# Performance work log

Hardware: AMD Instinct MI355X
Metric: run time of the kernel (lower is better)

Reference implementation:

```python
import jax, jax.numpy as jnp
import numpy as np

REC_W, COMMIT_W, SMOOTH_W = 1.0, 1.0, 0.1
CHUNK_SIZE = 10
W_DEC = 5
EPS = 1e-12


def conv1d(x, w, b):
    # x: (B, Cin, T), w: (Cout, Cin, K) -> 'same' padding, stride 1
    p = (w.shape[-1] - 1) // 2
    y = jax.lax.conv_general_dilated(x, w, (1,), [(p, p)],
                                     dimension_numbers=("NCH", "OIH", "NCH"))
    return y + b[None, :, None]


def adaptive_avg_pool1d(x, out_size):
    # PyTorch adaptive_avg_pool1d: bin i averages input[start:end],
    # start = floor(i*In/Out), end = ceil((i+1)*In/Out). Via cumsum.
    In = x.shape[-1]
    i = jnp.arange(out_size)
    start = (i * In) // out_size
    end = -((-(i + 1) * In) // out_size)
    cs = jnp.concatenate([jnp.zeros_like(x[..., :1]), jnp.cumsum(x, -1)], -1)
    return (cs[..., end] - cs[..., start]) / (end - start).astype(x.dtype)


def interp_linear(x, out_size):
    # F.interpolate(mode='linear', align_corners=False)
    In = x.shape[-1]
    scale = In / out_size
    src = jnp.maximum((jnp.arange(out_size) + 0.5) * scale - 0.5, 0.0)
    i0 = jnp.floor(src).astype(jnp.int32)
    i1 = jnp.minimum(i0 + 1, In - 1)
    frac = (src - i0).astype(x.dtype)
    return x[..., i0] * (1 - frac) + x[..., i1] * frac


def rotate_to(src, tgt):
    # rotation trick (vector-quantize-pytorch): Householder-style rotation of src onto tgt direction
    sg = jax.lax.stop_gradient
    ns = jnp.linalg.norm(src, axis=-1, keepdims=True)
    nt = jnp.linalg.norm(tgt, axis=-1, keepdims=True)
    u = src / (ns + EPS)
    q = tgt / (nt + EPS)
    w = sg((u + q) / (jnp.linalg.norm(u + q, axis=-1, keepdims=True) + EPS))
    e = src
    rotated = (e
               - 2 * jnp.sum(e * w, -1, keepdims=True) * w
               + 2 * jnp.sum(e * sg(u), -1, keepdims=True) * q)
    return rotated * sg(nt / (ns + EPS))


def residual_vq(x, codebooks):
    # x: (B, T, D); codebooks: (Q, K, D)
    sg = jax.lax.stop_gradient
    residual = x
    quantized_out = jnp.zeros_like(x)
    codes, losses = [], []
    for qi in range(codebooks.shape[0]):
        cb = codebooks[qi]                                # (K, D)
        d = (jnp.sum(residual * residual, -1, keepdims=True)
             - 2.0 * jnp.einsum("btd,kd->btk", residual, cb)
             + jnp.sum(cb * cb, -1)[None, None, :])       # (B, T, K)
        idx = jnp.argmin(d, axis=-1)                      # (B, T)
        quant = cb[idx]                                   # (B, T, D)
        losses.append(jnp.mean((sg(quant) - residual) ** 2))  # commitment loss
        quant_r = rotate_to(residual, quant)
        quantized_out = quantized_out + quant_r
        residual = residual - sg(quant_r)
        codes.append(idx)
    return quantized_out, jnp.stack(codes, -1), jnp.stack(losses)


def setup_inputs() -> dict:
    key = jax.random.key(0)
    ks = jax.random.split(key, 16)
    B, T = 16, 8000
    input_dim, hidden, latent, K, Q = 2, 512, 128, 1024, 4
    s = 0.02
    return {
        "traj_xy": jax.random.normal(ks[0], (B, input_dim, T), jnp.float32),
        "masks": jnp.ones((B, T), jnp.bool_),
        "enc1_w": s * jax.random.normal(ks[1], (hidden, input_dim * CHUNK_SIZE, 3), jnp.float32),
        "enc1_b": jnp.zeros((hidden,), jnp.float32),
        "enc2a_w": s * jax.random.normal(ks[2], (hidden, hidden, 5), jnp.float32),
        "enc2a_b": jnp.zeros((hidden,), jnp.float32),
        "enc2b_w": s * jax.random.normal(ks[3], (latent, hidden, 7), jnp.float32),
        "enc2b_b": jnp.zeros((latent,), jnp.float32),
        "dec1_w": s * jax.random.normal(ks[4], (hidden, latent + Q, 5), jnp.float32),
        "dec1_b": jnp.zeros((hidden,), jnp.float32),
        "dec2_w": s * jax.random.normal(ks[5], (latent, hidden, 3), jnp.float32),
        "dec2_b": jnp.zeros((latent,), jnp.float32),
        "codebooks": jax.random.normal(ks[6], (Q, K, latent), jnp.float32),
    }


def _forward(traj_xy, enc1_w, enc1_b, enc2a_w, enc2a_b, enc2b_w, enc2b_b,
             dec1_w, dec1_b, dec2_w, dec2_b, codebooks):
    B, D, T = traj_xy.shape
    Tn = T // CHUNK_SIZE
    # (B, D, T) -> (B, D*chunk, T/chunk)
    x = traj_xy.reshape(B, D, Tn, CHUNK_SIZE).transpose(0, 2, 1, 3).reshape(B, Tn, D * CHUNK_SIZE)
    x = x.transpose(0, 2, 1)
    z = jax.nn.relu(conv1d(x, enc1_w, enc1_b))
    z = adaptive_avg_pool1d(z, T // 2)
    z = interp_linear(z, T)
    z = jax.nn.relu(conv1d(z, enc2a_w, enc2a_b))
    z = conv1d(z, enc2b_w, enc2b_b)           # (B, latent, T)
    z_e = z.transpose(0, 2, 1)                # (B, T, latent)

    quantized, codes, vq_losses = residual_vq(z_e, codebooks)
    vq_loss = jnp.mean(vq_losses)

    codes_z = codes.transpose(0, 2, 1).astype(z.dtype)   # (B, Q, T)
    quant = quantized.transpose(0, 2, 1)                 # (B, latent, T)

    # chunked decoder loop, vectorized: starts t = 0, W, ..., T-2W
    Wd = W_DEC
    count = (T - 2 * Wd) // Wd + 1                       # = T/W - 1
    span = count * Wd                                    # = T - W
    Lq, Qn = quant.shape[1], codes_z.shape[1]
    past = quant[:, :, :span].reshape(B, Lq, count, Wd)
    cq = codes_z[:, :, :span].reshape(B, Qn, count, Wd)
    dec_in = jnp.concatenate([past, cq], axis=1)         # (B, Lq+Q, count, W)
    dec_in = dec_in.transpose(0, 2, 1, 3).reshape(B * count, Lq + Qn, Wd)
    h = jax.nn.relu(conv1d(dec_in, dec1_w, dec1_b))
    dec_out = conv1d(h, dec2_w, dec2_b)                  # (B*count, latent, W)
    true_chunk = quant[:, :, Wd:Wd + span].reshape(B, Lq, count, Wd)
    true_chunk = true_chunk.transpose(0, 2, 1, 3).reshape(B * count, Lq, Wd)
    recon_loss = jnp.mean((dec_out - true_chunk) ** 2)   # mean of equal-size per-chunk MSEs

    c0 = codes[:, :, 0]
    smooth_loss = jnp.mean((c0[:, 1:] != c0[:, :-1]).astype(z.dtype))

    loss = recon_loss * REC_W + vq_loss * COMMIT_W + smooth_loss * SMOOTH_W
    return codes, loss, recon_loss, vq_loss, smooth_loss


def reference(traj_xy, masks, enc1_w, enc1_b, enc2a_w, enc2a_b, enc2b_w, enc2b_b,
              dec1_w, dec1_b, dec2_w, dec2_b, codebooks):
    return _forward(traj_xy, enc1_w, enc1_b, enc2a_w, enc2a_b, enc2b_w, enc2b_b,
                    dec1_w, dec1_b, dec2_w, dec2_b, codebooks)
```

## Files before the change

kernel.cpp:

```cpp
#include <hip/hip_runtime.h>
#include <cstdint>
#include <cstddef>

#define B_     16
#define T_     8000
#define TN_    800
#define HID_   512
#define L_     128
#define KCB_   1024
#define Q_     4
#define COUNT_ 1599
#define NC_    (B_*COUNT_)
#define NTOK_  (B_*T_)
#define EPSF   1e-12

#define KP1_   672
#define NN1_   2560
#define KP2_   2560
#define NN2_   640

#define ZROWS_ 8072
#define ZROWU_ 1024
#define Z2ROWS_ 8072ull
#define Z2ROWU_ 1024ull
// ... 327 lines not shown
        #pragma unroll
        for (int j = 0; j < 4; ++j) acc[i][j] = (f32x4){0.f,0.f,0.f,0.f};

    for (int ci0 = 0; ci0 < 512; ci0 += 32){
        __syncthreads();
        for (int idx = tid; idx < 1056; idx += 256){
            int row = idx >> 3, rem = idx & 7, pl = rem >> 2, qo = rem & 3;
            *(uint4*)&SH[pl*4224 + row*32 + qo*8] =
                *(const uint4*)&Zb[(size_t)(t0 + row)*ZROWU_ + (size_t)pl*512 + ci0 + qo*8];
        }
        for (int u = 0; u < 5; ++u){
            if (u) __syncthreads();
            #pragma unroll
            for (int p = 0; p < 4; ++p){
                int idx = p*256 + tid;
                int n = idx >> 3, rem = idx & 7, pl = rem >> 2, qo = rem & 3;
                *(uint4*)&SH[8448 + pl*4096 + n*32 + qo*8] =
                    *(const uint4*)&Wp[((size_t)(co0+n)*2 + pl)*2560 + u*512 + ci0 + qo*8];
            }
            __syncthreads();
            s16x8 w[2][4], z[2][4];
            #pragma unroll
            for (int pl = 0; pl < 2; ++pl)
                #pragma unroll
                for (int mi = 0; mi < 4; ++mi)
                    w[pl][mi] = *(const s16x8*)&SH[8448 + pl*4096 + (wr*64 + mi*16 + lr)*32 + lg*8];
            #pragma unroll
            for (int pl = 0; pl < 2; ++pl)
                #pragma unroll
                for (int ni = 0; ni < 4; ++ni)
                    z[pl][ni] = *(const s16x8*)&SH[pl*4224 + (wc*64 + ni*16 + lr + u)*32 + lg*8];
            #pragma unroll
            for (int mi = 0; mi < 4; ++mi)
                #pragma unroll
                for (int ni = 0; ni < 4; ++ni){
                    f32x4 c = acc[mi][ni];
                    c = MFMA16(w[0][mi], z[0][ni], c);
                    c = MFMA16(w[0][mi], z[1][ni], c);
                    c = MFMA16(w[1][mi], z[0][ni], c);
                    acc[mi][ni] = c;
                }
        }
    }
    unsigned short* Zo = z2t + (size_t)lb*(Z2ROWS_*Z2ROWU_);
    #pragma unroll
    for (int pl = 0; pl < 2; ++pl){
        __syncthreads();
        #pragma unroll
        for (int mi = 0; mi < 4; ++mi){
            int cb = wr*64 + mi*16 + lg*4;
            #pragma unroll
            for (int ni = 0; ni < 4; ++ni){
                int tl = wc*64 + ni*16 + lr;
                #pragma unroll
                for (int r = 0; r < 4; ++r){
                    float v = fmaxf(acc[mi][ni][r] + bias[co0 + cb + r], 0.f);
                    unsigned short h, l; bsplit(v, h, l);
                    SH[tl*136 + cb + r] = pl ? l : h;
                }
            }
        }
        __syncthreads();
        int tl = tid >> 1, half = tid & 1;
        if (t0 + tl < T_){
            uint4* dst = (uint4*)&Zo[((size_t)(t0 + tl + 3))*Z2ROWU_ + (size_t)pl*512 + co0 + half*64];
            const uint4* src = (const uint4*)&SH[tl*136 + half*64];
            #pragma unroll
            for (int e = 0; e < 8; ++e) dst[e] = src[e];
        }
    }
}

__global__ __launch_bounds__(256) void k_mconv2b(const unsigned short* __restrict__ Z2,
                                                 const unsigned short* __restrict__ Wp,
                                                 const float* __restrict__ bias,
                                                 float* __restrict__ ze){
    __shared__ unsigned short SH[12672];
    int lb = blockIdx.y;
    int t0 = blockIdx.x * 64;
    int tid = threadIdx.x;
    int lane = tid & 63, wid = tid >> 6;
    int lr = lane & 15, lg = lane >> 4;
    const unsigned short* Zb = Z2 + (size_t)lb*(Z2ROWS_*Z2ROWU_);
    f32x4 acc[2][4];
    #pragma unroll
    for (int i = 0; i < 2; ++i)
        #pragma unroll
        for (int j = 0; j < 4; ++j) acc[i][j] = (f32x4){0.f,0.f,0.f,0.f};

    for (int ci0 = 0; ci0 < 512; ci0 += 32){
        __syncthreads();
        for (int idx = tid; idx < 560; idx += 256){
            int row = idx >> 3, rem = idx & 7, pl = rem >> 2, qo = rem & 3;
            *(uint4*)&SH[pl*2240 + row*32 + qo*8] =
                *(const uint4*)&Zb[(size_t)(t0 + row)*Z2ROWU_ + (size_t)pl*512 + ci0 + qo*8];
        }
        for (int u = 0; u < 7; ++u){
            if (u) __syncthreads();
            #pragma unroll
            for (int p = 0; p < 4; ++p){
                int idx = p*256 + tid;
                int n = idx >> 3, rem = idx & 7, pl = rem >> 2, qo = rem & 3;
                *(uint4*)&SH[4480 + pl*4096 + n*32 + qo*8] =
                    *(const uint4*)&Wp[((size_t)n*2 + pl)*3584 + u*512 + ci0 + qo*8];
            }
            __syncthreads();
            s16x8 w[2][2], z[2][4];
            #pragma unroll
            for (int pl = 0; pl < 2; ++pl)
                #pragma unroll
                for (int mi = 0; mi < 2; ++mi)
                    w[pl][mi] = *(const s16x8*)&SH[4480 + pl*4096 + (wid*32 + mi*16 + lr)*32 + lg*8];
            #pragma unroll
            for (int pl = 0; pl < 2; ++pl)
                #pragma unroll
                for (int ni = 0; ni < 4; ++ni)
                    z[pl][ni] = *(const s16x8*)&SH[pl*2240 + (ni*16 + lr + u)*32 + lg*8];
            #pragma unroll
            for (int mi = 0; mi < 2; ++mi)
                #pragma unroll
                for (int ni = 0; ni < 4; ++ni){
                    f32x4 c = acc[mi][ni];
                    c = MFMA16(w[0][mi], z[0][ni], c);
                    c = MFMA16(w[0][mi], z[1][ni], c);
                    c = MFMA16(w[1][mi], z[0][ni], c);
                    acc[mi][ni] = c;
                }
        }
    }
    #pragma unroll
    for (int mi = 0; mi < 2; ++mi){
        int cb = wid*32 + mi*16 + lg*4;
        float4 bv = *(const float4*)&bias[cb];
        #pragma unroll
        for (int ni = 0; ni < 4; ++ni){
            int t = t0 + ni*16 + lr;
            float4 o;
            o.x = acc[mi][ni][0] + bv.x;
            o.y = acc[mi][ni][1] + bv.y;
            o.z = acc[mi][ni][2] + bv.z;
            o.w = acc[mi][ni][3] + bv.w;
            *(float4*)&ze[((size_t)lb*T_ + t)*L_ + cb] = o;
        }
    }
}

__global__ __launch_bounds__(256) void k_mgemm1(const unsigned short* __restrict__ Ap,
                                                const unsigned short* __restrict__ Bp,
                                                const float* __restrict__ bias,
                                                unsigned short* __restrict__ Hp){
    __shared__ unsigned short AL[2][128][40];
    __shared__ unsigned short BL[2][128][40];
    int m0 = blockIdx.x * 128, n0 = blockIdx.y * 128;
    int tid = threadIdx.x;
    int lane = tid & 63, wid = tid >> 6;
    int wr = wid >> 1, wc = wid & 1;
    int lr = lane & 15, lg = lane >> 4;
    f32x4 acc[4][4];
    #pragma unroll
    for (int i = 0; i < 4; ++i)
        #pragma unroll
        for (int j = 0; j < 4; ++j) acc[i][j] = (f32x4){0.f,0.f,0.f,0.f};

    for (int kb = 0; kb < KP1_; kb += 32){
        __syncthreads();
        #pragma unroll
        for (int p = 0; p < 4; ++p){
            int slot = p*256 + tid;
            int m = slot >> 3, pl = (slot >> 2) & 1, q = slot & 3;
            uint4 v = *(const uint4*)&Ap[((size_t)(m0+m)*2 + pl)*KP1_ + kb + q*8];
            *(uint4*)&AL[pl][m][q*8] = v;
        }
        #pragma unroll
        for (int p = 0; p < 4; ++p){
            int slot = p*256 + tid;
            int n = slot >> 3, pl = (slot >> 2) & 1, q = slot & 3;
            uint4 v = *(const uint4*)&Bp[((size_t)(n0+n)*2 + pl)*KP1_ + kb + q*8];
            *(uint4*)&BL[pl][n][q*8] = v;
        }
        __syncthreads();
        s16x8 a[2][4], b[2][4];
        #pragma unroll
        for (int pl = 0; pl < 2; ++pl)
            #pragma unroll
            for (int mi = 0; mi < 4; ++mi)
                a[pl][mi] = *(const s16x8*)&AL[pl][wr*64 + mi*16 + lr][lg*8];
        #pragma unroll
        for (int pl = 0; pl < 2; ++pl)
            #pragma unroll
            for (int ni = 0; ni < 4; ++ni)
                b[pl][ni] = *(const s16x8*)&BL[pl][wc*64 + ni*16 + lr][lg*8];
        #pragma unroll
        for (int mi = 0; mi < 4; ++mi)
            #pragma unroll
            for (int ni = 0; ni < 4; ++ni){
                f32x4 c = acc[mi][ni];
                c = MFMA16(a[0][mi], b[0][ni], c);
                c = MFMA16(a[0][mi], b[1][ni], c);
                c = MFMA16(a[1][mi], b[0][ni], c);
                acc[mi][ni] = c;
            }
    }
    #pragma unroll
    for (int mi = 0; mi < 4; ++mi){
        int mbase = m0 + wr*64 + mi*16 + lg*4;
        #pragma unroll
        for (int ni = 0; ni < 4; ++ni){
            int n = n0 + wc*64 + ni*16 + lr;
            float bv = bias[n/5];
            #pragma unroll
            for (int r = 0; r < 4; ++r){
                float v = fmaxf(acc[mi][ni][r] + bv, 0.f);
                unsigned short h, l; bsplit(v, h, l);
                size_t m = (size_t)(mbase + r);
                Hp[(m*2 + 0)*NN1_ + n] = h;
                Hp[(m*2 + 1)*NN1_ + n] = l;
            }
        }
    }
}

__global__ __launch_bounds__(256) void k_mgemm2rec(const unsigned short* __restrict__ Ap,
                                                   const unsigned short* __restrict__ Bp,
                                                   const float* __restrict__ bias,
                                                   const float* __restrict__ zeq, float* __restrict__ scal,
                                                   int M, int m0g){
    __shared__ unsigned short AL[2][128][40];
    __shared__ unsigned short BL[2][128][40];
    int m0 = blockIdx.x * 128, n0 = blockIdx.y * 128;
    int tid = threadIdx.x;
    int lane = tid & 63, wid = tid >> 6;
    int wr = wid >> 1, wc = wid & 1;
    int lr = lane & 15, lg = lane >> 4;
    f32x4 acc[4][4];
    #pragma unroll
    for (int i = 0; i < 4; ++i)
        #pragma unroll
        for (int j = 0; j < 4; ++j) acc[i][j] = (f32x4){0.f,0.f,0.f,0.f};

    for (int kb = 0; kb < KP2_; kb += 32){
        __syncthreads();
        #pragma unroll
        for (int p = 0; p < 4; ++p){
            int slot = p*256 + tid;
            int m = slot >> 3, pl = (slot >> 2) & 1, q = slot & 3;
            uint4 v = *(const uint4*)&Ap[((size_t)(m0+m)*2 + pl)*KP2_ + kb + q*8];
            *(uint4*)&AL[pl][m][q*8] = v;
        }
        #pragma unroll
        for (int p = 0; p < 4; ++p){
            int slot = p*256 + tid;
            int n = slot >> 3, pl = (slot >> 2) & 1, q = slot & 3;
            uint4 v = *(const uint4*)&Bp[((size_t)(n0+n)*2 + pl)*KP2_ + kb + q*8];
            *(uint4*)&BL[pl][n][q*8] = v;
        }
        __syncthreads();
        s16x8 a[2][4], b[2][4];
        #pragma unroll
        for (int pl = 0; pl < 2; ++pl)
            #pragma unroll
            for (int mi = 0; mi < 4; ++mi)
                a[pl][mi] = *(const s16x8*)&AL[pl][wr*64 + mi*16 + lr][lg*8];
        #pragma unroll
        for (int pl = 0; pl < 2; ++pl)
            #pragma unroll
            for (int ni = 0; ni < 4; ++ni)
                b[pl][ni] = *(const s16x8*)&BL[pl][wc*64 + ni*16 + lr][lg*8];
        #pragma unroll
        for (int mi = 0; mi < 4; ++mi)
            #pragma unroll
            for (int ni = 0; ni < 4; ++ni){
                f32x4 c = acc[mi][ni];
                c = MFMA16(a[0][mi], b[0][ni], c);
                c = MFMA16(a[0][mi], b[1][ni], c);
                c = MFMA16(a[1][mi], b[0][ni], c);
                acc[mi][ni] = c;
            }
    }
    float lsum = 0.f;
    #pragma unroll
    for (int mi = 0; mi < 4; ++mi){
        #pragma unroll
        for (int r = 0; r < 4; ++r){
            int ml = wr*64 + mi*16 + lg*4 + r;
            int mlg = m0 + ml;
            if (mlg >= M) continue;
            int gm = m0g + mlg;
            int b = gm / COUNT_, c = gm % COUNT_;
            const float* tgtB = zeq + ((size_t)b*T_ + (size_t)(c+1)*5) * L_;
            #pragma unroll
            for (int ni = 0; ni < 4; ++ni){
                int n = n0 + wc*64 + ni*16 + lr;
                int co = n / 5, t = n % 5;
                float v = acc[mi][ni][r] + bias[co];
                float d = v - tgtB[(size_t)t*L_ + co];
                lsum += d*d;
            }
        }
    }
    lsum = wred(lsum);
    if (lane == 0) atomicAdd(&scal[1024 + ((blockIdx.x*5 + blockIdx.y) & 255)], lsum);
}

#define RF(j) rf[tok*132 + sub*33 + (j)]
__global__ __launch_bounds__(256, 2) void k_vqfuse(float* __restrict__ ze,
                                                   const unsigned short* __restrict__ cbp,
                                                   const double* __restrict__ cnorm,
                                                   const float* __restrict__ cnf,
                                                   const float* __restrict__ cb,
                                                   int* __restrict__ codes,
                                                   float* __restrict__ scal){
    __shared__ unsigned short rb[2][64][136];
    __shared__ float rf[64*132];
    __shared__ float mvS[4][64][2];
    __shared__ int   miS[4][64][2];
    int tok0 = blockIdx.x * 64;
    int tid = threadIdx.x;
    int lane = tid & 63, wv = tid >> 6;
    int lr = lane & 15, lg = lane >> 4;
    int tok = tid >> 2, sub = tid & 3, dbase = sub*32;
    {
        const float* zp = &ze[((size_t)(tok0 + tok))*L_ + dbase];
        #pragma unroll
        for (int h = 0; h < 8; ++h){
            float4 v = *(const float4*)&zp[h*4];
            RF(h*4+0)=v.x; RF(h*4+1)=v.y; RF(h*4+2)=v.z; RF(h*4+3)=v.w;
        }
    }
    for (int q = 0; q < Q_; ++q){
        #pragma unroll
        for (int j = 0; j < 4; ++j){
            unsigned hp[4], lp[4];
            #pragma unroll
            for (int e = 0; e < 4; ++e){
                unsigned short h0,l0,h1,l1;
                bsplit(RF(j*8+e*2+0), h0, l0);
                bsplit(RF(j*8+e*2+1), h1, l1);
                hp[e] = (unsigned)h0 | ((unsigned)h1 << 16);
                lp[e] = (unsigned)l0 | ((unsigned)l1 << 16);
            }
            *(uint4*)&rb[0][tok][dbase + j*8] = make_uint4(hp[0],hp[1],hp[2],hp[3]);
            *(uint4*)&rb[1][tok][dbase + j*8] = make_uint4(lp[0],lp[1],lp[2],lp[3]);
        }
        __syncthreads();
        const unsigned short* cq = cbp + (size_t)q*(2*16*1024*8);
        const float* cnq = cnf + (size_t)q*KCB_;
        int code0w = wv*256;
        float m1[4], m2[4]; int i1[4], i2[4];
        #pragma unroll
        for (int t = 0; t < 4; ++t){ m1[t]=3.4e38f; m2[t]=3.4e38f; i1[t]=0x7fffffff; i2[t]=0x7fffffff; }
        for (int ch = 0; ch < 8; ++ch){
            f32x4 acc[2][4];
            #pragma unroll
            for (int i = 0; i < 2; ++i)
                #pragma unroll
                for (int j = 0; j < 4; ++j) acc[i][j] = (f32x4){0.f,0.f,0.f,0.f};
            #pragma unroll
            for (int ks = 0; ks < 4; ++ks){
                s16x8 b0[4], b1[4];
                #pragma unroll
                for (int tf = 0; tf < 4; ++tf){
                    b0[tf] = *(const s16x8*)&rb[0][tf*16 + lr][ks*32 + lg*8];
                    b1[tf] = *(const s16x8*)&rb[1][tf*16 + lr][ks*32 + lg*8];
                }
                #pragma unroll
                for (int mi = 0; mi < 2; ++mi){
                    s16x8 a0 = *(const s16x8*)&cq[((size_t)(0*16 + ks*4 + lg)*1024
                                                   + code0w + ch*32 + mi*16 + lr)*8];
                    s16x8 a1 = *(const s16x8*)&cq[((size_t)(1*16 + ks*4 + lg)*1024
                                                   + code0w + ch*32 + mi*16 + lr)*8];
                    #pragma unroll
                    for (int tf = 0; tf < 4; ++tf){
                        f32x4 c = acc[mi][tf];
                        c = MFMA16(a0, b0[tf], c);
                        c = MFMA16(a0, b1[tf], c);
                        c = MFMA16(a1, b0[tf], c);
                        acc[mi][tf] = c;
                    }
                }
            }
            #pragma unroll
            for (int mi = 0; mi < 2; ++mi){
                float4 cn4 = *(const float4*)&cnq[code0w + ch*32 + mi*16 + lg*4];
                float cnv[4] = {cn4.x, cn4.y, cn4.z, cn4.w};
                #pragma unroll
                for (int tf = 0; tf < 4; ++tf)
                    #pragma unroll
                    for (int rr = 0; rr < 4; ++rr){
                        float sc = cnv[rr] - 2.f*acc[mi][tf][rr];
                        int code = code0w + ch*32 + mi*16 + lg*4 + rr;
                        bool c1 = sc < m1[tf];
                        bool c2 = sc < m2[tf];
                        if (c1){ m2[tf]=m1[tf]; i2[tf]=i1[tf]; m1[tf]=sc; i1[tf]=code; }
                        else if (c2){ m2[tf]=sc; i2[tf]=code; }
                    }
            }
        }
        #pragma unroll
        for (int tf = 0; tf < 4; ++tf){
            float a1 = m1[tf], a2 = m2[tf]; int ai1 = i1[tf], ai2 = i2[tf];
            #pragma unroll
            for (int m = 16; m <= 32; m <<= 1){
                float o1 = __shfl_xor(a1, m), o2 = __shfl_xor(a2, m);
                int oi1 = __shfl_xor(ai1, m), oi2 = __shfl_xor(ai2, m);
                bool sw = (o1 < a1) || (o1 == a1 && oi1 < ai1);
                float w1 = sw ? o1 : a1;  int wi1 = sw ? oi1 : ai1;
                float l1 = sw ? a1 : o1;  int li1 = sw ? ai1 : oi1;
                float w2 = sw ? o2 : a2;  int wi2 = sw ? oi2 : ai2;
                bool s2 = (l1 < w2) || (l1 == w2 && li1 < wi2);
                a1 = w1; ai1 = wi1;
                a2 = s2 ? l1 : w2; ai2 = s2 ? li1 : wi2;
            }
            if (lg == 0){
                mvS[wv][tf*16 + lr][0] = a1; mvS[wv][tf*16 + lr][1] = a2;
                miS[wv][tf*16 + lr][0] = ai1; miS[wv][tf*16 + lr][1] = ai2;
            }
        }
        __syncthreads();
        float a1 = mvS[0][tok][0], a2 = mvS[0][tok][1];
        int ai1 = miS[0][tok][0], ai2 = miS[0][tok][1];
        #pragma unroll
        for (int w = 1; w < 4; ++w){
            float o1 = mvS[w][tok][0], o2 = mvS[w][tok][1];
            int oi1 = miS[w][tok][0], oi2 = miS[w][tok][1];
            bool sw = (o1 < a1) || (o1 == a1 && oi1 < ai1);
            float w1 = sw ? o1 : a1;  int wi1 = sw ? oi1 : ai1;
            float l1 = sw ? a1 : o1;  int li1 = sw ? ai1 : oi1;
            float w2 = sw ? o2 : a2;  int wi2 = sw ? oi2 : ai2;
            bool s2 = (l1 < w2) || (l1 == w2 && li1 < wi2);
            a1 = w1; ai1 = wi1;
            a2 = s2 ? l1 : w2; ai2 = s2 ? li1 : wi2;
        }
        int id = ai1;
        int idb = (a2 - a1 < 0.1f) ? ai2 : -1;

        const float* cbq  = cb + (size_t)q*KCB_*L_;
        const double* cnq64 = cnorm + (size_t)q*KCB_;
        if (idb >= 0){
            const float* c1p = cbq + (size_t)id * L_ + dbase;
            const float* c2p = cbq + (size_t)idb * L_ + dbase;
            double p1 = 0.0, p2 = 0.0;
            #pragma unroll
            for (int h = 0; h < 8; ++h){
                float4 a4 = *(const float4*)&c1p[h*4];
                float4 b4 = *(const float4*)&c2p[h*4];
                float ca[4] = {a4.x,a4.y,a4.z,a4.w};
                float cbv[4] = {b4.x,b4.y,b4.z,b4.w};
                #pragma unroll
                for (int e = 0; e < 4; ++e){
                    double rv = (double)RF(h*4 + e);
                    p1 = fma(rv, (double)ca[e], p1);
                    p2 = fma(rv, (double)cbv[e], p2);
                }
            }
            p1 = qred(p1); p2 = qred(p2);
            double d1 = cnq64[id]  - 2.0*p1;
            double d2 = cnq64[idb] - 2.0*p2;
            if (d2 < d1 || (d2 == d1 && idb < id)) id = idb;
        }
        if (sub == 0) codes[((size_t)(tok0 + tok))*Q_ + q] = id;

        const float* cp = cbq + (size_t)id * L_ + dbase;
        double srr = 0.0, scc = 0.0, src = 0.0;
        #pragma unroll
        for (int h = 0; h < 8; ++h){
            float4 c4 = *(const float4*)&cp[h*4];
            float cvs[4] = {c4.x,c4.y,c4.z,c4.w};
            #pragma unroll
            for (int e = 0; e < 4; ++e){
                double rd = (double)RF(h*4 + e);
                double cd = (double)cvs[e];
                srr = fma(rd, rd, srr);
                scc = fma(cd, cd, scc);
                src = fma(rd, cd, src);
            }
        }
        srr = qred(srr); scc = qred(scc); src = qred(src);
        double ns = sqrt(srr), nt = sqrt(scc);
        double insp = 1.0/(ns + EPSF), intp = 1.0/(nt + EPSF);
        double sn2 = srr*insp*insp + 2.0*src*insp*intp + scc*intp*intp;
        double isn = 1.0/(sqrt(sn2) + EPSF);
        double ew = (srr*insp + src*intp)*isn;
        double eu = srr*insp;
        double scale = nt*insp;
        double clp = 0.0;
        #pragma unroll
        for (int h = 0; h < 8; ++h){
            float4 c4 = *(const float4*)&cp[h*4];
            float cvs[4] = {c4.x,c4.y,c4.z,c4.w};
            #pragma unroll
            for (int e = 0; e < 4; ++e){
                int s = h*4 + e;
                float rf32 = RF(s);
                double rv = (double)rf32, cd = (double)cvs[e];
                double wd = (rv*insp + cd*intp)*isn;
                double qd = cd*intp;
                float qr = (float)((rv - 2.0*ew*wd + 2.0*eu*qd)*scale);
                RF(s) = rf32 - qr;
                float dd = cvs[e] - rf32;
                clp += (double)(dd*dd);
            }
        }
        clp = qred(clp);
        double cl = (sub == 0) ? clp : 0.0;
        cl = wredd(cl);
        if ((tid & 63) == 0) atomicAdd(&scal[q*256 + (blockIdx.x & 255)], (float)cl);
        __syncthreads();
    }
    float* zw = &ze[((size_t)(tok0 + tok))*L_ + dbase];
    #pragma unroll
    for (int h = 0; h < 8; ++h){
        float4 o = *(float4*)&zw[h*4];
        o.x -= RF(h*4+0);
        o.y -= RF(h*4+1);
        o.z -= RF(h*4+2);
        o.w -= RF(h*4+3);
        *(float4*)&zw[h*4] = o;
    }
}

__global__ __launch_bounds__(256) void k_smooth(const int* __restrict__ codes, float* __restrict__ scal){
    int i = blockIdx.x*256 + threadIdx.x;
    float v = 0.f;
    if (i < B_*(T_-1)){
        int b = i / (T_-1), t = i % (T_-1);
        int c0 = codes[((size_t)b*T_ + t)*Q_];
        int c1 = codes[((size_t)b*T_ + t + 1)*Q_];
        v = (c0 != c1) ? 1.f : 0.f;
    }
    v = wred(v);
    if ((threadIdx.x & 63) == 0) atomicAdd(&scal[1280 + (blockIdx.x & 255)], v);
}

__global__ __launch_bounds__(256) void k_builda1b(const float* __restrict__ zeq,
                                                  const int* __restrict__ codes, unsigned short* __restrict__ A1,
                                                  int m0, int M, int Mpad){
    int i = blockIdx.x*256 + threadIdx.x;
    if (i >= Mpad*KP1_) return;
    int ml = i / KP1_, k = i % KP1_;
    float v = 0.f;
    if (ml < M && k < 660){
        int u = k / 132, ci = k % 132;
        int gm = m0 + ml;
        int b = gm / COUNT_, c = gm % COUNT_;
        int t = c*5 + u;
        if (ci < L_) v = zeq[((size_t)b*T_ + t)*L_ + ci];
        else         v = (float)codes[((size_t)b*T_ + t)*Q_ + (ci - L_)];
    }
    unsigned short h, l; bsplit(v, h, l);
    A1[((size_t)ml*2 + 0)*KP1_ + k] = h;
    A1[((size_t)ml*2 + 1)*KP1_ + k] = l;
}

__global__ __launch_bounds__(256) void k_codesout(const int* __restrict__ codes, float* __restrict__ out){
    int i = blockIdx.x*256 + threadIdx.x;
    if (i < NTOK_*Q_) out[i] = (float)codes[i];
}

__global__ __launch_bounds__(64) void k_final(const float* __restrict__ scal, float* __restrict__ out){
    if (threadIdx.x != 0) return;
    double s[4] = {0,0,0,0};
    double rec = 0, sm = 0;
    for (int i = 0; i < 256; ++i){
        s[0] += scal[i]; s[1] += scal[256+i]; s[2] += scal[512+i]; s[3] += scal[768+i];
        rec += scal[1024+i]; sm += scal[1280+i];
    }
    double denom = 16384000.0;
    double vq = (s[0]/denom + s[1]/denom + s[2]/denom + s[3]/denom) / 4.0;
    double recon = rec / 16373760.0;
    double smooth = sm / 127984.0;
    double loss = recon + vq + 0.1*smooth;
    out[512000] = (float)loss;
    out[512001] = (float)recon;
    out[512002] = (float)vq;
    out[512003] = (float)smooth;
}

extern "C" void kernel_launch(void* const* d_in, const int* in_sizes, int n_in,
                              void* d_out, int out_size, void* d_ws, size_t ws_size,
                              hipStream_t stream) {
    const float* traj = (const float*)d_in[0];
    const float* e1w  = (const float*)d_in[2];
    const float* e1b  = (const float*)d_in[3];
    const float* e2aw = (const float*)d_in[4];
    const float* e2ab = (const float*)d_in[5];
    const float* e2bw = (const float*)d_in[6];
    const float* e2bb = (const float*)d_in[7];
    const float* d1w  = (const float*)d_in[8];
    const float* d1b  = (const float*)d_in[9];
    const float* d2w  = (const float*)d_in[10];
    const float* d2b  = (const float*)d_in[11];
    const float* cbks = (const float*)d_in[12];
    float* out = (float*)d_out;
    float* ws  = (float*)d_ws;
    int* codes_i = (int*)(ws + OFF_CODES);
    double* cnormd = (double*)(ws + OFF_CNORM);

    size_t wsf = ws_size / 4;
    size_t avail = (wsf > OFF_SCR) ? (wsf - OFF_SCR) : 0;
    int bc = 16;
    while (bc > 1 && (size_t)bc * 8675328ull > avail) bc >>= 1;
    long long mc_ll = (long long)(avail / 3232ull);
    int mc = (int)((mc_ll / 128) * 128);
    if (mc < 128) mc = 128;
    if (mc > 12800) mc = 12800;

    k_zero<<<8, 256, 0, stream>>>(ws + OFF_SCAL);
    k_wtrans<<<(30720+255)/256, 256, 0, stream>>>(e1w,  ws + OFF_WT1,  20,  3, 512, 30720);
    k_wprep2a<<<(512*2560+255)/256, 256, 0, stream>>>(e2aw, (unsigned short*)(ws + OFF_WT2A));
    k_wprep2b<<<(128*3584+255)/256, 256, 0, stream>>>(e2bw, (unsigned short*)(ws + OFF_WT2B));
    k_wexpand2a<<<(NN1_*KP1_+255)/256, 256, 0, stream>>>(d1w, (unsigned short*)(ws + OFF_W1E));
    k_wexpand2<<<(NN2_*KP2_+255)/256, 256, 0, stream>>>(d2w, (unsigned short*)(ws + OFF_W2E), 512, 3, KP2_, NN2_*KP2_);
    k_cbprep<<<16, 256, 0, stream>>>(cbks, (unsigned short*)(ws + OFF_CBT), cnormd, ws + OFF_CNF);
    k_buildx<<<(256000+255)/256, 256, 0, stream>>>(traj, ws + OFF_X1);

    float* z1c  = ws + OFF_SCR;
    float* zupf = z1c + (size_t)bc * 409600;
    float* z2tf = zupf + (size_t)bc * 4132864;
    k_zpad2<<<(bc*9216+255)/256, 256, 0, stream>>>((unsigned short*)z2tf, bc);
    for (int b0 = 0; b0 < B_; b0 += bc){
        k_conv<3, true, false, 128><<<dim3(7, 4, bc), 256, 0, stream>>>(
            ws + OFF_X1 + (size_t)b0*20*TN_, ws + OFF_WT1, e1b, z1c, 20, 512, TN_);
        k_cumsum<<<(bc*512+63)/64, 64, 0, stream>>>(z1c, bc*512);
        k_upT<<<dim3((ZROWS_*512)/256, bc), 256, 0, stream>>>(z1c, (unsigned short*)zupf);
        k_mconv2a<<<dim3(63, 4, bc), 256, 0, stream>>>(
            (const unsigned short*)zupf, (const unsigned short*)(ws + OFF_WT2A), e2ab,
            (unsigned short*)z2tf);
        k_mconv2b<<<dim3(125, bc), 256, 0, stream>>>(
            (const unsigned short*)z2tf, (const unsigned short*)(ws + OFF_WT2B), e2bb,
            ws + OFF_ZE + (size_t)b0*T_*L_);
    }

    k_vqfuse<<<NTOK_/64, 256, 0, stream>>>(
        ws + OFF_ZE, (const unsigned short*)(ws + OFF_CBT), cnormd, ws + OFF_CNF,
        cbks, codes_i, ws + OFF_SCAL);

    k_smooth<<<(B_*(T_-1)+255)/256, 256, 0, stream>>>(codes_i, ws + OFF_SCAL);

    float* A1c = ws + OFF_SCR;
    float* Hc  = A1c + (size_t)mc * KP1_;
    for (int m0 = 0; m0 < NC_; m0 += mc){
        int M = (NC_ - m0 < mc) ? (NC_ - m0) : mc;
        int Mpad = ((M + 127) / 128) * 128;
        k_builda1b<<<(Mpad*KP1_+255)/256, 256, 0, stream>>>(ws + OFF_ZE, codes_i,
                                                            (unsigned short*)A1c, m0, M, Mpad);
        k_mgemm1<<<dim3(Mpad/128, NN1_/128), 256, 0, stream>>>(
            (const unsigned short*)A1c, (const unsigned short*)(ws + OFF_W1E), d1b,
            (unsigned short*)Hc);
        k_mgemm2rec<<<dim3(Mpad/128, NN2_/128), 256, 0, stream>>>(
            (const unsigned short*)Hc, (const unsigned short*)(ws + OFF_W2E), d2b,
            ws + OFF_ZE, ws + OFF_SCAL, M, m0);
    }

    k_codesout<<<(NTOK_*Q_+255)/256, 256, 0, stream>>>(codes_i, out);
    k_final<<<1, 64, 0, stream>>>(ws + OFF_SCAL, out);
    (void)in_sizes; (void)n_in; (void)out_size; (void)ws_size;
}
```

Before: 3.447 ms.

## Split fused residual VQ kernel into per-stage screen and rotate kernels

The single fused VQ kernel, which looped over all four codebooks with the residual held in shared memory, becomes a copy kernel plus a per-codebook pair of launches: an MFMA top-2 screening kernel that writes candidates to global memory, and a rotation/refinement kernel that keeps the residual in registers and writes it back. This frees the shared-memory residual buffer and separates the MFMA-heavy phase from the double-precision rotation phase, which may improve occupancy and per-kernel scheduling. In exchange it adds eight extra launches and repeated global round trips of the 64 MB residual plus the top-2 buffer.

```diff
diff --git a/kernel.cpp b/kernel.cpp
--- a/kernel.cpp
+++ b/kernel.cpp
@@ -653,16 +653,16 @@
     if (lane == 0) atomicAdd(&scal[1024 + ((blockIdx.x*5 + blockIdx.y) & 255)], lsum);
 }
 
-#define RF(j) rf[tok*132 + sub*33 + (j)]
-__global__ __launch_bounds__(256, 2) void k_vqfuse(float* __restrict__ ze,
-                                                   const unsigned short* __restrict__ cbp,
-                                                   const double* __restrict__ cnorm,
-                                                   const float* __restrict__ cnf,
-                                                   const float* __restrict__ cb,
-                                                   int* __restrict__ codes,
-                                                   float* __restrict__ scal){
+__global__ __launch_bounds__(256) void k_vqcopy(const float* __restrict__ src, float* __restrict__ dst){
+    size_t i = ((size_t)blockIdx.x*256 + threadIdx.x)*4;
+    *(float4*)&dst[i] = *(const float4*)&src[i];
+}
+
+__global__ __launch_bounds__(256, 2) void k_vqscreen(const float* __restrict__ resid,
+                                                     const unsigned short* __restrict__ cbp,
+                                                     const float* __restrict__ cnf,
+                                                     float* __restrict__ top2, int q){
     __shared__ unsigned short rb[2][64][136];
-    __shared__ float rf[64*132];
     __shared__ float mvS[4][64][2];
     __shared__ int   miS[4][64][2];
     int tok0 = blockIdx.x * 64;
@@ -671,109 +671,86 @@
     int lr = lane & 15, lg = lane >> 4;
     int tok = tid >> 2, sub = tid & 3, dbase = sub*32;
     {
-        const float* zp = &ze[((size_t)(tok0 + tok))*L_ + dbase];
-        #pragma unroll
-        for (int h = 0; h < 8; ++h){
-            float4 v = *(const float4*)&zp[h*4];
-            RF(h*4+0)=v.x; RF(h*4+1)=v.y; RF(h*4+2)=v.z; RF(h*4+3)=v.w;
-        }
-    }
-    for (int q = 0; q < Q_; ++q){
+        const float* zp = &resid[((size_t)(tok0 + tok))*L_ + dbase];
         #pragma unroll
         for (int j = 0; j < 4; ++j){
+            float4 va = *(const float4*)&zp[j*8];
+            float4 vb = *(const float4*)&zp[j*8 + 4];
+            float rv[8] = {va.x,va.y,va.z,va.w, vb.x,vb.y,vb.z,vb.w};
             unsigned hp[4], lp[4];
             #pragma unroll
             for (int e = 0; e < 4; ++e){
                 unsigned short h0,l0,h1,l1;
-                bsplit(RF(j*8+e*2+0), h0, l0);
-                bsplit(RF(j*8+e*2+1), h1, l1);
+                bsplit(rv[e*2+0], h0, l0);
+                bsplit(rv[e*2+1], h1, l1);
                 hp[e] = (unsigned)h0 | ((unsigned)h1 << 16);
                 lp[e] = (unsigned)l0 | ((unsigned)l1 << 16);
             }
             *(uint4*)&rb[0][tok][dbase + j*8] = make_uint4(hp[0],hp[1],hp[2],hp[3]);
             *(uint4*)&rb[1][tok][dbase + j*8] = make_uint4(lp[0],lp[1],lp[2],lp[3]);
         }
-        __syncthreads();
-        const unsigned short* cq = cbp + (size_t)q*(2*16*1024*8);
-        const float* cnq = cnf + (size_t)q*KCB_;
-        int code0w = wv*256;
-        float m1[4], m2[4]; int i1[4], i2[4];
-        #pragma unroll
-        for (int t = 0; t < 4; ++t){ m1[t]=3.4e38f; m2[t]=3.4e38f; i1[t]=0x7fffffff; i2[t]=0x7fffffff; }
-        for (int ch = 0; ch < 8; ++ch){
-            f32x4 acc[2][4];
-            #pragma unroll
-            for (int i = 0; i < 2; ++i)
-                #pragma unroll
-                for (int j = 0; j < 4; ++j) acc[i][j] = (f32x4){0.f,0.f,0.f,0.f};
-            #pragma unroll
-            for (int ks = 0; ks < 4; ++ks){
-                s16x8 b0[4], b1[4];
+    }
+    __syncthreads();
+    const unsigned short* cq = cbp + (size_t)q*(2*16*1024*8);
+    const float* cnq = cnf + (size_t)q*KCB_;
+    int code0w = wv*256;
+    float m1[4], m2[4]; int i1[4], i2[4];
+    #pragma unroll
+    for (int t = 0; t < 4; ++t){ m1[t]=3.4e38f; m2[t]=3.4e38f; i1[t]=0x7fffffff; i2[t]=0x7fffffff; }
+    for (int ch = 0; ch < 8; ++ch){
+        f32x4 acc[2][4];
+        #pragma unroll
+        for (int i = 0; i < 2; ++i)
+            #pragma unroll
+            for (int j = 0; j < 4; ++j) acc[i][j] = (f32x4){0.f,0.f,0.f,0.f};
+        #pragma unroll
+        for (int ks = 0; ks < 4; ++ks){
+            s16x8 b0[4], b1[4];
+            #pragma unroll
+            for (int tf = 0; tf < 4; ++tf){
+                b0[tf] = *(const s16x8*)&rb[0][tf*16 + lr][ks*32 + lg*8];
+                b1[tf] = *(const s16x8*)&rb[1][tf*16 + lr][ks*32 + lg*8];
+            }
+            #pragma unroll
+            for (int mi = 0; mi < 2; ++mi){
+                s16x8 a0 = *(const s16x8*)&cq[((size_t)(0*16 + ks*4 + lg)*1024
+                                               + code0w + ch*32 + mi*16 + lr)*8];
+                s16x8 a1 = *(const s16x8*)&cq[((size_t)(1*16 + ks*4 + lg)*1024
+                                               + code0w + ch*32 + mi*16 + lr)*8];
                 #pragma unroll
                 for (int tf = 0; tf < 4; ++tf){
-                    b0[tf] = *(const s16x8*)&rb[0][tf*16 + lr][ks*32 + lg*8];
-                    b1[tf] = *(const s16x8*)&rb[1][tf*16 + lr][ks*32 + lg*8];
+                    f32x4 c = acc[mi][tf];
+                    c = MFMA16(a0, b0[tf], c);
+                    c = MFMA16(a0, b1[tf], c);
+                    c = MFMA16(a1, b0[tf], c);
+                    acc[mi][tf] = c;
                 }
+            }
+        }
+        #pragma unroll
+        for (int mi = 0; mi < 2; ++mi){
+            float4 cn4 = *(const float4*)&cnq[code0w + ch*32 + mi*16 + lg*4];
+            float cnv[4] = {cn4.x, cn4.y, cn4.z, cn4.w};
+            #pragma unroll
+            for (int tf = 0; tf < 4; ++tf)
                 #pragma unroll
-                for (int mi = 0; mi < 2; ++mi){
-                    s16x8 a0 = *(const s16x8*)&cq[((size_t)(0*16 + ks*4 + lg)*1024
-                                                   + code0w + ch*32 + mi*16 + lr)*8];
-                    s16x8 a1 = *(const s16x8*)&cq[((size_t)(1*16 + ks*4 + lg)*1024
-                                                   + code0w + ch*32 + mi*16 + lr)*8];
-                    #pragma unroll
-                    for (int tf = 0; tf < 4; ++tf){
-                        f32x4 c = acc[mi][tf];
-                        c = MFMA16(a0, b0[tf], c);
-                        c = MFMA16(a0, b1[tf], c);
-                        c = MFMA16(a1, b0[tf], c);
-                        acc[mi][tf] = c;
-                    }
+                for (int rr = 0; rr < 4; ++rr){
+                    float sc = cnv[rr] - 2.f*acc[mi][tf][rr];
+                    int code = code0w + ch*32 + mi*16 + lg*4 + rr;
+                    bool c1 = sc < m1[tf];
+                    bool c2 = sc < m2[tf];
+                    if (c1){ m2[tf]=m1[tf]; i2[tf]=i1[tf]; m1[tf]=sc; i1[tf]=code; }
+                    else if (c2){ m2[tf]=sc; i2[tf]=code; }
                 }
-            }
-            #pragma unroll
-            for (int mi = 0; mi < 2; ++mi){
-                float4 cn4 = *(const float4*)&cnq[code0w + ch*32 + mi*16 + lg*4];
-                float cnv[4] = {cn4.x, cn4.y, cn4.z, cn4.w};
-                #pragma unroll
-                for (int tf = 0; tf < 4; ++tf)
-                    #pragma unroll
-                    for (int rr = 0; rr < 4; ++rr){
-                        float sc = cnv[rr] - 2.f*acc[mi][tf][rr];
-                        int code = code0w + ch*32 + mi*16 + lg*4 + rr;
-                        bool c1 = sc < m1[tf];
-                        bool c2 = sc < m2[tf];
-                        if (c1){ m2[tf]=m1[tf]; i2[tf]=i1[tf]; m1[tf]=sc; i1[tf]=code; }
-                        else if (c2){ m2[tf]=sc; i2[tf]=code; }
-                    }
-            }
-        }
-        #pragma unroll
-        for (int tf = 0; tf < 4; ++tf){
-            float a1 = m1[tf], a2 = m2[tf]; int ai1 = i1[tf], ai2 = i2[tf];
-            #pragma unroll
-            for (int m = 16; m <= 32; m <<= 1){
-                float o1 = __shfl_xor(a1, m), o2 = __shfl_xor(a2, m);
-                int oi1 = __shfl_xor(ai1, m), oi2 = __shfl_xor(ai2, m);
-                bool sw = (o1 < a1) || (o1 == a1 && oi1 < ai1);
-                float w1 = sw ? o1 : a1;  int wi1 = sw ? oi1 : ai1;
-                float l1 = sw ? a1 : o1;  int li1 = sw ? ai1 : oi1;
-                float w2 = sw ? o2 : a2;  int wi2 = sw ? oi2 : ai2;
-                bool s2 = (l1 < w2) || (l1 == w2 && li1 < wi2);
-                a1 = w1; ai1 = wi1;
-                a2 = s2 ? l1 : w2; ai2 = s2 ? li1 : wi2;
-            }
-            if (lg == 0){
-                mvS[wv][tf*16 + lr][0] = a1; mvS[wv][tf*16 + lr][1] = a2;
-                miS[wv][tf*16 + lr][0] = ai1; miS[wv][tf*16 + lr][1] = ai2;
-            }
-        }
-        __syncthreads();
-        float a1 = mvS[0][tok][0], a2 = mvS[0][tok][1];
-        int ai1 = miS[0][tok][0], ai2 = miS[0][tok][1];
-        #pragma unroll
-        for (int w = 1; w < 4; ++w){
-            float o1 = mvS[w][tok][0], o2 = mvS[w][tok][1];
-            int oi1 = miS[w][tok][0], oi2 = miS[w][tok][1];
+        }
+    }
+    #pragma unroll
+    for (int tf = 0; tf < 4; ++tf){
+        float a1 = m1[tf], a2 = m2[tf]; int ai1 = i1[tf], ai2 = i2[tf];
+        #pragma unroll
+        for (int m = 16; m <= 32; m <<= 1){
+            float o1 = __shfl_xor(a1, m), o2 = __shfl_xor(a2, m);
+            int oi1 = __shfl_xor(ai1, m), oi2 = __shfl_xor(ai2, m);
             bool sw = (o1 < a1) || (o1 == a1 && oi1 < ai1);
             float w1 = sw ? o1 : a1;  int wi1 = sw ? oi1 : ai1;
             float l1 = sw ? a1 : o1;  int li1 = sw ? ai1 : oi1;
@@ -782,91 +759,143 @@
             a1 = w1; ai1 = wi1;
             a2 = s2 ? l1 : w2; ai2 = s2 ? li1 : wi2;
         }
-        int id = ai1;
-        int idb = (a2 - a1 < 0.1f) ? ai2 : -1;
-
-        const float* cbq  = cb + (size_t)q*KCB_*L_;
-        const double* cnq64 = cnorm + (size_t)q*KCB_;
-        if (idb >= 0){
-            const float* c1p = cbq + (size_t)id * L_ + dbase;
-            const float* c2p = cbq + (size_t)idb * L_ + dbase;
-            double p1 = 0.0, p2 = 0.0;
-            #pragma unroll
-            for (int h = 0; h < 8; ++h){
-                float4 a4 = *(const float4*)&c1p[h*4];
-                float4 b4 = *(const float4*)&c2p[h*4];
-                float ca[4] = {a4.x,a4.y,a4.z,a4.w};
-                float cbv[4] = {b4.x,b4.y,b4.z,b4.w};
-                #pragma unroll
-                for (int e = 0; e < 4; ++e){
-                    double rv = (double)RF(h*4 + e);
-                    p1 = fma(rv, (double)ca[e], p1);
-                    p2 = fma(rv, (double)cbv[e], p2);
-                }
-            }
-            p1 = qred(p1); p2 = qred(p2);
-            double d1 = cnq64[id]  - 2.0*p1;
-            double d2 = cnq64[idb] - 2.0*p2;
-            if (d2 < d1 || (d2 == d1 && idb < id)) id = idb;
-        }
-        if (sub == 0) codes[((size_t)(tok0 + tok))*Q_ + q] = id;
-
-        const float* cp = cbq + (size_t)id * L_ + dbase;
-        double srr = 0.0, scc = 0.0, src = 0.0;
+        if (lg == 0){
+            mvS[wv][tf*16 + lr][0] = a1; mvS[wv][tf*16 + lr][1] = a2;
+            miS[wv][tf*16 + lr][0] = ai1; miS[wv][tf*16 + lr][1] = ai2;
+        }
+    }
+    __syncthreads();
+    if (tid < 64){
+        float a1 = mvS[0][tid][0], a2 = mvS[0][tid][1];
+        int ai1 = miS[0][tid][0], ai2 = miS[0][tid][1];
+        #pragma unroll
+        for (int w = 1; w < 4; ++w){
+            float o1 = mvS[w][tid][0], o2 = mvS[w][tid][1];
+            int oi1 = miS[w][tid][0], oi2 = miS[w][tid][1];
+            bool sw = (o1 < a1) || (o1 == a1 && oi1 < ai1);
+            float w1 = sw ? o1 : a1;  int wi1 = sw ? oi1 : ai1;
+            float l1 = sw ? a1 : o1;  int li1 = sw ? ai1 : oi1;
+            float w2 = sw ? o2 : a2;  int wi2 = sw ? oi2 : ai2;
+            bool s2 = (l1 < w2) || (l1 == w2 && li1 < wi2);
+            a1 = w1; ai1 = wi1;
+            a2 = s2 ? l1 : w2; ai2 = s2 ? li1 : wi2;
+        }
+        float* t2 = &top2[((size_t)(tok0 + tid))*4];
+        t2[0] = a1; t2[1] = a2;
+        ((int*)t2)[2] = ai1; ((int*)t2)[3] = ai2;
+    }
+}
+
+__global__ __launch_bounds__(256, 2) void k_vqrot(float* __restrict__ ze, float* __restrict__ resid,
+                                                  const float* __restrict__ top2,
+                                                  const double* __restrict__ cnorm,
+                                                  const float* __restrict__ cb,
+                                                  int* __restrict__ codes, float* __restrict__ scal,
+                                                  int q, int last){
+    int tok0 = blockIdx.x * 64;
+    int tid = threadIdx.x;
+    int tok = tid >> 2, sub = tid & 3, dbase = sub*32;
+    float r[32];
+    {
+        const float* zp = &resid[((size_t)(tok0 + tok))*L_ + dbase];
         #pragma unroll
         for (int h = 0; h < 8; ++h){
-            float4 c4 = *(const float4*)&cp[h*4];
-            float cvs[4] = {c4.x,c4.y,c4.z,c4.w};
+            float4 v = *(const float4*)&zp[h*4];
+            r[h*4+0]=v.x; r[h*4+1]=v.y; r[h*4+2]=v.z; r[h*4+3]=v.w;
+        }
+    }
+    const float* t2 = &top2[((size_t)(tok0 + tok))*4];
+    float a1 = t2[0], a2 = t2[1];
+    int id = ((const int*)t2)[2];
+    int idb = (a2 - a1 < 0.1f) ? ((const int*)t2)[3] : -1;
+
+    const float* cbq  = cb + (size_t)q*KCB_*L_;
+    const double* cnq64 = cnorm + (size_t)q*KCB_;
+    if (idb >= 0){
+        const float* c1p = cbq + (size_t)id * L_ + dbase;
+        const float* c2p = cbq + (size_t)idb * L_ + dbase;
+        double p1 = 0.0, p2 = 0.0;
+        #pragma unroll
+        for (int h = 0; h < 8; ++h){
+            float4 a4 = *(const float4*)&c1p[h*4];
+            float4 b4 = *(const float4*)&c2p[h*4];
+            float ca[4] = {a4.x,a4.y,a4.z,a4.w};
+            float cbv[4] = {b4.x,b4.y,b4.z,b4.w};
             #pragma unroll
             for (int e = 0; e < 4; ++e){
-                double rd = (double)RF(h*4 + e);
-                double cd = (double)cvs[e];
-                srr = fma(rd, rd, srr);
-                scc = fma(cd, cd, scc);
-                src = fma(rd, cd, src);
-            }
-        }
-        srr = qred(srr); scc = qred(scc); src = qred(src);
-        double ns = sqrt(srr), nt = sqrt(scc);
-        double insp = 1.0/(ns + EPSF), intp = 1.0/(nt + EPSF);
-        double sn2 = srr*insp*insp + 2.0*src*insp*intp + scc*intp*intp;
-        double isn = 1.0/(sqrt(sn2) + EPSF);
-        double ew = (srr*insp + src*intp)*isn;
-        double eu = srr*insp;
-        double scale = nt*insp;
-        double clp = 0.0;
+                double rv = (double)r[h*4 + e];
+                p1 = fma(rv, (double)ca[e], p1);
+                p2 = fma(rv, (double)cbv[e], p2);
+            }
+        }
+        p1 = qred(p1); p2 = qred(p2);
+        double d1 = cnq64[id]  - 2.0*p1;
+        double d2 = cnq64[idb] - 2.0*p2;
+        if (d2 < d1 || (d2 == d1 && idb < id)) id = idb;
+    }
+    if (sub == 0) codes[((size_t)(tok0 + tok))*Q_ + q] = id;
+
+    const float* cp = cbq + (size_t)id * L_ + dbase;
+    double srr = 0.0, scc = 0.0, src = 0.0;
+    #pragma unroll
+    for (int h = 0; h < 8; ++h){
+        float4 c4 = *(const float4*)&cp[h*4];
+        float cvs[4] = {c4.x,c4.y,c4.z,c4.w};
+        #pragma unroll
+        for (int e = 0; e < 4; ++e){
+            double rd = (double)r[h*4 + e];
+            double cd = (double)cvs[e];
+            srr = fma(rd, rd, srr);
+            scc = fma(cd, cd, scc);
+            src = fma(rd, cd, src);
+        }
+    }
+    srr = qred(srr); scc = qred(scc); src = qred(src);
+    double ns = sqrt(srr), nt = sqrt(scc);
+    double insp = 1.0/(ns + EPSF), intp = 1.0/(nt + EPSF);
+    double sn2 = srr*insp*insp + 2.0*src*insp*intp + scc*intp*intp;
+    double isn = 1.0/(sqrt(sn2) + EPSF);
+    double ew = (srr*insp + src*intp)*isn;
+    double eu = srr*insp;
+    double scale = nt*insp;
+    double clp = 0.0;
+    #pragma unroll
+    for (int h = 0; h < 8; ++h){
+        float4 c4 = *(const float4*)&cp[h*4];
+        float cvs[4] = {c4.x,c4.y,c4.z,c4.w};
+        #pragma unroll
+        for (int e = 0; e < 4; ++e){
+            float rf32 = r[h*4 + e];
+            double rv = (double)rf32, cd = (double)cvs[e];
+            double wd = (rv*insp + cd*intp)*isn;
+            double qd = cd*intp;
+            float qr = (float)((rv - 2.0*ew*wd + 2.0*eu*qd)*scale);
+            r[h*4 + e] = rf32 - qr;
+            float dd = cvs[e] - rf32;
+            clp += (double)(dd*dd);
+        }
+    }
+    clp = qred(clp);
+    double cl = (sub == 0) ? clp : 0.0;
+    cl = wredd(cl);
+    if ((tid & 63) == 0) atomicAdd(&scal[q*256 + (blockIdx.x & 255)], (float)cl);
+
+    if (!last){
+        float* rp = &resid[((size_t)(tok0 + tok))*L_ + dbase];
+        #pragma unroll
+        for (int h = 0; h < 8; ++h)
+            *(float4*)&rp[h*4] = make_float4(r[h*4+0], r[h*4+1], r[h*4+2], r[h*4+3]);
+    } else {
+        float* zw = &ze[((size_t)(tok0 + tok))*L_ + dbase];
         #pragma unroll
         for (int h = 0; h < 8; ++h){
-            float4 c4 = *(const float4*)&cp[h*4];
-            float cvs[4] = {c4.x,c4.y,c4.z,c4.w};
-            #pragma unroll
-            for (int e = 0; e < 4; ++e){
-                int s = h*4 + e;
-                float rf32 = RF(s);
-                double rv = (double)rf32, cd = (double)cvs[e];
-                double wd = (rv*insp + cd*intp)*isn;
-                double qd = cd*intp;
-                float qr = (float)((rv - 2.0*ew*wd + 2.0*eu*qd)*scale);
-                RF(s) = rf32 - qr;
-                float dd = cvs[e] - rf32;
-                clp += (double)(dd*dd);
-            }
-        }
-        clp = qred(clp);
-        double cl = (sub == 0) ? clp : 0.0;
-        cl = wredd(cl);
-        if ((tid & 63) == 0) atomicAdd(&scal[q*256 + (blockIdx.x & 255)], (float)cl);
-        __syncthreads();
-    }
-    float* zw = &ze[((size_t)(tok0 + tok))*L_ + dbase];
-    #pragma unroll
-    for (int h = 0; h < 8; ++h){
-        float4 o = *(float4*)&zw[h*4];
-        o.x -= RF(h*4+0);
-        o.y -= RF(h*4+1);
-        o.z -= RF(h*4+2);
-        o.w -= RF(h*4+3);
-        *(float4*)&zw[h*4] = o;
+            float4 o = *(float4*)&zw[h*4];
+            o.x -= r[h*4+0];
+            o.y -= r[h*4+1];
+            o.z -= r[h*4+2];
+            o.w -= r[h*4+3];
+            *(float4*)&zw[h*4] = o;
+        }
     }
 }
 
@@ -982,9 +1011,16 @@
             ws + OFF_ZE + (size_t)b0*T_*L_);
     }
 
-    k_vqfuse<<<NTOK_/64, 256, 0, stream>>>(
-        ws + OFF_ZE, (const unsigned short*)(ws + OFF_CBT), cnormd, ws + OFF_CNF,
-        cbks, codes_i, ws + OFF_SCAL);
+    float* residG = ws + OFF_SCR;
+    float* top2G  = residG + 16384000ull;
+    k_vqcopy<<<16000, 256, 0, stream>>>(ws + OFF_ZE, residG);
+    for (int q = 0; q < Q_; ++q){
+        k_vqscreen<<<NTOK_/64, 256, 0, stream>>>(
+            residG, (const unsigned short*)(ws + OFF_CBT), ws + OFF_CNF, top2G, q);
+        k_vqrot<<<NTOK_/64, 256, 0, stream>>>(
+            ws + OFF_ZE, residG, top2G, cnormd, cbks, codes_i, ws + OFF_SCAL,
+            q, (q == Q_-1) ? 1 : 0);
+    }
 
     k_smooth<<<(B_*(T_-1)+255)/256, 256, 0, stream>>>(codes_i, ws + OFF_SCAL);
 
```

Result: no change. 3.435 ms (-0.3%).
